# Kernel optimization log

Measured on AMD Instinct MI355X. Metric: run time of the kernel, lower is better.

Reference implementation:

```python
import jax, jax.numpy as jnp
import numpy as np

B, S, DM, NH, WIN = 2, 2048, 1024, 16, 256
DH = DM // NH          # 64
DFF = 4 * DM           # 4096
WIDTHS = (256, 512, 1024)  # 1024 == hidden -> identity (no adapter in torch ModuleDict)


def _ln(x, g, b, eps=1e-5):
    m = jnp.mean(x, -1, keepdims=True)
    v = jnp.var(x, -1, keepdims=True)
    return (x - m) * jax.lax.rsqrt(v + eps) * g + b


def _gelu(t):
    return jax.nn.gelu(t, approximate=False)  # torch nn.GELU default = exact erf


def setup_inputs() -> dict:
    key = jax.random.key(0)
    ks = iter(jax.random.split(key, 32))

    def lin(fi, fo):
        # xavier_uniform(gain=1/sqrt(2)) ~ scale sqrt(2/(fi+fo))/sqrt(2); normal init is fine for a numeric reference
        std = float((1.0 / np.sqrt(2.0)) * np.sqrt(2.0 / (fi + fo)))
        return (jax.random.normal(next(ks), (fi, fo), jnp.float32) * std,
                jnp.zeros((fo,), jnp.float32))

    inp = {}
    inp['x'] = jax.random.normal(next(ks), (B, S, DM), jnp.float32)
    inp['width_multiplier'] = jax.random.uniform(next(ks), (B, S, 1), jnp.float32)
    # attention projections
    inp['wq'], inp['bq'] = lin(DM, DM)
    inp['wk'], inp['bk'] = lin(DM, DM)
    inp['wv'], inp['bv'] = lin(DM, DM)
    inp['wo'], inp['bo'] = lin(DM, DM)
    inp['lnq_g'] = jnp.ones((DH,), jnp.float32); inp['lnq_b'] = jnp.zeros((DH,), jnp.float32)
    inp['lnk_g'] = jnp.ones((DH,), jnp.float32); inp['lnk_b'] = jnp.zeros((DH,), jnp.float32)
    # base FFN
    inp['fc1_w'], inp['fc1_b'] = lin(DM, DFF)
    inp['fc2_w'], inp['fc2_b'] = lin(DFF, DM)
    inp['lni_g'] = jnp.ones((DM,), jnp.float32); inp['lni_b'] = jnp.zeros((DM,), jnp.float32)
    inp['lnh_g'] = jnp.ones((DFF,), jnp.float32); inp['lnh_b'] = jnp.zeros((DFF,), jnp.float32)
    # width adapters (for widths != hidden_dim)
    inp['a256_w1'], inp['a256_b1'] = lin(DM, 256)
    inp['a256_w2'], inp['a256_b2'] = lin(256, DM)
    inp['a512_w1'], inp['a512_b1'] = lin(DM, 512)
    inp['a512_w2'], inp['a512_b2'] = lin(512, DM)
    # router output: index into WIDTHS per token
    inp['width_idx'] = jax.random.randint(next(ks), (B, S), 0, 3)
    return inp


def reference(x, width_multiplier, wq, bq, wk, bk, wv, bv, wo, bo,
              lnq_g, lnq_b, lnk_g, lnk_b, fc1_w, fc1_b, fc2_w, fc2_b,
              lni_g, lni_b, lnh_g, lnh_b,
              a256_w1, a256_b1, a256_w2, a256_b2,
              a512_w1, a512_b1, a512_w2, a512_b2, width_idx):
    # ---- local causal windowed attention pathway ----
    q = (x @ wq + bq).reshape(B, S, NH, DH)
    k = (x @ wk + bk).reshape(B, S, NH, DH)
    v = (x @ wv + bv).reshape(B, S, NH, DH)
    q = _ln(q, lnq_g, lnq_b)  # per-head-dim LayerNorm (torch ln_q on [B,S,H,Dh])
    k = _ln(k, lnk_g, lnk_b)
    scores = jnp.einsum('bihd,bjhd->bhij', q, k) / np.float32(np.sqrt(DH))
    ii = jnp.arange(S)[:, None]
    jj = jnp.arange(S)[None, :]
    allowed = (jj <= ii) & (ii - jj <= WIN)  # causal + local window
    scores = jnp.where(allowed[None, None], scores, -jnp.inf)
    probs = jax.nn.softmax(scores, axis=-1)
    attn = jnp.einsum('bhij,bjhd->bihd', probs, v).reshape(B, S, DM)
    h = x + attn @ wo + bo  # residual around attention pathway

    # ---- width-adaptive FFN ----
    xn = _ln(h, lni_g, lni_b)
    hid = _ln(_gelu(xn @ fc1_w + fc1_b), lnh_g, lnh_b)
    base = hid @ fc2_w + fc2_b
    # per-width adapters, combined by routing mask (dense compute, masked scatter)
    a0 = _gelu(xn @ a256_w1 + a256_b1) @ a256_w2 + a256_b2
    a1 = _gelu(xn @ a512_w1 + a512_b1) @ a512_w2 + a512_b2
    a2 = xn  # width == hidden_dim -> identity pass-through
    m0 = (width_idx == 0)[..., None]
    m1 = (width_idx == 1)[..., None]
    m2 = (width_idx == 2)[..., None]
    adaptive = jnp.where(m0, a0, 0.0) + jnp.where(m1, a1, 0.0) + jnp.where(m2, a2, 0.0)
    ffn_out = base * width_multiplier + adaptive * (1.0 - width_multiplier)
    return h + ffn_out
```

## Files before the change

### kernel.cpp

```cpp
#include <hip/hip_runtime.h>
#include <math.h>

#define B_   2
#define S_   2048
#define DM_  1024
#define NH_  16
#define DH_  64
#define DFF_ 4096
#define WIN_ 256
#define MTOK (B_*S_)

typedef unsigned short ushort_t;
typedef short s16x8 __attribute__((ext_vector_type(8)));
typedef float f32x4 __attribute__((ext_vector_type(4)));

__device__ __forceinline__ float b2f(ushort_t u) {
    union { unsigned int i; float f; } c; c.i = ((unsigned int)u) << 16; return c.f;
}
__device__ __forceinline__ ushort_t f2b(float f) {
    union { float f; unsigned int i; } c; c.f = f;
    unsigned int r = c.i + 0x7fffu + ((c.i >> 16) & 1u);
    return (ushort_t)(r >> 16);
}
__device__ __forceinline__ float gelu_fast(float x) {
    const float u = 0.7978845608f * x * fmaf(0.044715f, x * x, 1.0f);
    const float e = __expf(2.0f * u);
    const float t = 1.0f - 2.0f / (e + 1.0f);
    return 0.5f * x * (1.0f + t);
}
__device__ __forceinline__ void gload16(const void* g, void* l) {
    __builtin_amdgcn_global_load_lds(
        (const __attribute__((address_space(1))) unsigned int*)g,
        (__attribute__((address_space(3))) unsigned int*)l, 16, 0, 0);
}
__device__ __forceinline__ int xcd_swz(int wgid, int nwg) {
    const int nx = 8;
    const int q = nwg / nx, r = nwg % nx;
    const int xcd = wgid % nx, lo = wgid / nx;
    const int base = (xcd < r) ? xcd * (q + 1) : r * (q + 1) + (xcd - r) * q;
    return base + lo;
}

__device__ __forceinline__ void gemm_loop(
    const ushort_t* __restrict__ A, int lda,
    const ushort_t* __restrict__ Bt, int ldb,
    int Kc, int bx, int by, f32x4 (&acc)[4][4])
{
    __shared__ __align__(16) ushort_t As[2][256 * 32];
    __shared__ __align__(16) ushort_t Bs[2][128 * 32];

    const int tid  = threadIdx.x;
    const int lane = tid & 63;
    const int w    = tid >> 6;
    const int row0 = by * 256;
    const int col0 = bx * 128;

    const int srow = lane >> 2;
    const int sk   = (lane & 3) * 8;
    const int wr   = (w >> 1) * 64;
    const int wc   = (w & 1) * 64;
    const int lr   = lane & 15;
    const int lk   = (lane >> 4) * 8;

    auto stage = [&](int buf, int k0) {
        #pragma unroll
        for (int i = 0; i < 2; ++i) {
            const int c = i * 8 + w;
            const int cr = c * 16 + srow;
            gload16(A + (size_t)(row0 + cr) * lda + k0 + sk,
                    (char*)As[buf] + c * 1024);
        }
        {
            const int cr = w * 16 + srow;
            gload16(Bt + (size_t)(col0 + cr) * ldb + k0 + sk,
                    (char*)Bs[buf] + w * 1024);
        }
    };

    const int nk = Kc >> 5;
    stage(0, 0);
    __syncthreads();
    int cur = 0;
    for (int k = 0; k < nk; ++k) {
        if (k + 1 < nk) stage(cur ^ 1, (k + 1) << 5);
        s16x8 af[4], bfr[4];
        #pragma unroll
        for (int mi = 0; mi < 4; ++mi)
            af[mi] = *(const s16x8*)&As[cur][(wr + mi * 16 + lr) * 32 + lk];
        #pragma unroll
        for (int ni = 0; ni < 4; ++ni)
            bfr[ni] = *(const s16x8*)&Bs[cur][(wc + ni * 16 + lr) * 32 + lk];
        #pragma unroll
        for (int mi = 0; mi < 4; ++mi)
            #pragma unroll
            for (int ni = 0; ni < 4; ++ni)
                acc[mi][ni] = __builtin_amdgcn_mfma_f32_16x16x32_bf16(
                    af[mi], bfr[ni], acc[mi][ni], 0, 0, 0);
        __syncthreads();
        cur ^= 1;
    }
}

__global__ __launch_bounds__(512) void gemm_qkvln(
    const ushort_t* __restrict__ A, const ushort_t* __restrict__ Bt,
    const float* __restrict__ bias,
    const float* __restrict__ qg, const float* __restrict__ qb,
    const float* __restrict__ kg, const float* __restrict__ kb,
    ushort_t* __restrict__ qh, ushort_t* __restrict__ kh, ushort_t* __restrict__ vh)
{
    f32x4 acc[4][4] = {};
    gemm_loop(A, 1024, Bt, 1024, 1024, blockIdx.x, blockIdx.y, acc);

    const int lane = threadIdx.x & 63;
    const int w    = threadIdx.x >> 6;
    const int wr   = (w >> 1) * 64;
    const int wc   = (w & 1) * 64;
    const int row0 = blockIdx.y * 256;
    const int col0 = blockIdx.x * 128;
    const int crow = (lane >> 4) * 4;
    const int ccol = lane & 15;
    const int sel  = (col0 + wc) >> 10;
    const int hh   = ((col0 + wc) & 1023) >> 6;
    ushort_t* dst = (sel == 0) ? qh : (sel == 1) ? kh : vh;

    #pragma unroll
    for (int mi = 0; mi < 4; ++mi) {
        float val[4][4];
        float s1[4] = {}, sq[4] = {};
        #pragma unroll
        for (int ni = 0; ni < 4; ++ni) {
            const float bc = bias[col0 + wc + ni * 16 + ccol];
            #pragma unroll
            for (int r = 0; r < 4; ++r) {
                const float v = acc[mi][ni][r] + bc;
                val[ni][r] = v;
                s1[r] += v;
                sq[r] = fmaf(v, v, sq[r]);
            }
        }
        if (sel < 2) {
            #pragma unroll
            for (int r = 0; r < 4; ++r) {
                #pragma unroll
                for (int m = 1; m < 16; m <<= 1) {
                    s1[r] += __shfl_xor(s1[r], m);
                    sq[r] += __shfl_xor(sq[r], m);
                }
            }
        }
        #pragma unroll
        for (int r = 0; r < 4; ++r) {
            const int r_abs = row0 + wr + mi * 16 + crow + r;
            const int bb = r_abs >> 11, ss = r_abs & 2047;
            const size_t db = (((size_t)(bb * NH_ + hh)) * S_ + ss) * 64;
            const float mean = s1[r] * 0.015625f;
            const float var  = sq[r] * 0.015625f - mean * mean;
            const float rstd = rsqrtf(var + 1e-5f);
            #pragma unroll
            for (int ni = 0; ni < 4; ++ni) {
                const int d = ni * 16 + ccol;
                float v = val[ni][r];
                if (sel == 0)      v = ((v - mean) * rstd * qg[d] + qb[d]) * 0.125f;
                else if (sel == 1) v = (v - mean) * rstd * kg[d] + kb[d];
                dst[db + d] = f2b(v);
            }
        }
    }
}

__global__ __launch_bounds__(512) void gemm_fc1ad(
    const ushort_t* __restrict__ A, const ushort_t* __restrict__ Bt,
    const float* __restrict__ bias,
    ushort_t* __restrict__ hid, ushort_t* __restrict__ tA)
{
    f32x4 acc[4][4] = {};
    gemm_loop(A, 1024, Bt, 1024, 1024, blockIdx.x, blockIdx.y, acc);

    const int lane = threadIdx.x & 63;
    const int w    = threadIdx.x >> 6;
    const int wr   = (w >> 1) * 64;
    const int wc   = (w & 1) * 64;
    const int row0 = blockIdx.y * 256;
    const int col0 = blockIdx.x * 128;
    const int crow = (lane >> 4) * 4;
    const int ccol = lane & 15;
    const bool isad = (col0 >= 4096);
    ushort_t* D = isad ? tA : hid;
    const int stride = isad ? 768 : 4096;
    const int cb     = isad ? 4096 : 0;

    #pragma unroll
    for (int ni = 0; ni < 4; ++ni) {
        const int col = col0 + wc + ni * 16 + ccol;
        const float bc = bias[col];
        #pragma unroll
        for (int mi = 0; mi < 4; ++mi) {
            #pragma unroll
            for (int r = 0; r < 4; ++r) {
                const int row = row0 + wr + mi * 16 + crow + r;
                D[(size_t)row * stride + (col - cb)] = f2b(gelu_fast(acc[mi][ni][r] + bc));
            }
        }
    }
}

__device__ __forceinline__ void epi_raw(
    f32x4 (&acc)[4][4], float* __restrict__ C, int N, int bx, int by)
{
    const int lane = threadIdx.x & 63;
    const int w    = threadIdx.x >> 6;
    const int wr   = (w >> 1) * 64;
    const int wc   = (w & 1) * 64;
    const int crow = (lane >> 4) * 4;
    const int ccol = lane & 15;
    #pragma unroll
    for (int ni = 0; ni < 4; ++ni) {
        const int col = bx * 128 + wc + ni * 16 + ccol;
        #pragma unroll
        for (int mi = 0; mi < 4; ++mi) {
            #pragma unroll
            for (int r = 0; r < 4; ++r) {
                const int row = by * 256 + wr + mi * 16 + crow + r;
                C[(size_t)row * N + col] = acc[mi][ni][r];
            }
        }
    }
}

__global__ __launch_bounds__(512) void gemm_wo_sk(
    const ushort_t* __restrict__ A, const ushort_t* __restrict__ Wt,
    float* __restrict__ p0, float* __restrict__ p1)
{
    const int z = blockIdx.z;
    f32x4 acc[4][4] = {};
    gemm_loop(A + z * 512, 1024, Wt + z * 512, 1024, 512, blockIdx.x, blockIdx.y, acc);
    epi_raw(acc, z ? p1 : p0, 1024, blockIdx.x, blockIdx.y);
}

__global__ __launch_bounds__(512) void gemm_fc2_sk(
    const ushort_t* __restrict__ A, const ushort_t* __restrict__ Bt,
    float* __restrict__ p0, float* __restrict__ p1)
{
    const int z = blockIdx.z;
    f32x4 acc[4][4] = {};
    gemm_loop(A + z * 2048, 4096, Bt + z * 2048, 4096, 2048, blockIdx.x, blockIdx.y, acc);
    epi_raw(acc, z ? p1 : p0, 1024, blockIdx.x, blockIdx.y);
}

__global__ __launch_bounds__(512) void gemm_adapters(
    const ushort_t* __restrict__ tA, const ushort_t* __restrict__ w2a,
    const ushort_t* __restrict__ w2b, const float* __restrict__ b2a,
    const float* __restrict__ b2b, float* __restrict__ a0, float* __restrict__ a1)
{
    const int z = blockIdx.z;
    const ushort_t* Ap = z ? tA + 256 : tA;
    const ushort_t* Wp = z ? w2b : w2a;
    const float*    bp = z ? b2b : b2a;
    float*          Cp = z ? a1 : a0;
    const int Kz = z ? 512 : 256;
    f32x4 acc[4][4] = {};
    gemm_loop(Ap, 768, Wp, Kz, Kz, blockIdx.x, blockIdx.y, acc);

    const int lane = threadIdx.x & 63;
    const int w    = threadIdx.x >> 6;
    const int wr   = (w >> 1) * 64;
    const int wc   = (w & 1) * 64;
    const int crow = (lane >> 4) * 4;
    const int ccol = lane & 15;
    #pragma unroll
    for (int ni = 0; ni < 4; ++ni) {
        const int col = blockIdx.x * 128 + wc + ni * 16 + ccol;
        const float bc = bp[col];
        #pragma unroll
        for (int mi = 0; mi < 4; ++mi) {
            #pragma unroll
            for (int r = 0; r < 4; ++r) {
                const int row = blockIdx.y * 256 + wr + mi * 16 + crow + r;
                Cp[(size_t)row * 1024 + col] = acc[mi][ni][r] + bc;
            }
        }
    }
}

__device__ __forceinline__ void wtrans_core(
    const float* __restrict__ W, ushort_t* __restrict__ Wt, int K, int N,
    int bx, int by)
{
    __shared__ float tile[32][33];
    const int n0 = bx * 32, k0 = by * 32;
    const int tx = threadIdx.x & 31, ty = threadIdx.x >> 5;
    #pragma unroll
    for (int j = 0; j < 4; ++j)
        tile[ty + j * 8][tx] = W[(size_t)(k0 + ty + j * 8) * N + n0 + tx];
    __syncthreads();
    #pragma unroll
    for (int j = 0; j < 4; ++j)
        Wt[(size_t)(n0 + ty + j * 8) * K + k0 + tx] = f2b(tile[tx][ty + j * 8]);
}

#define PREP_NBLK 17940
__global__ __launch_bounds__(256) void prep_all(
    const float* wq, const float* wk, const float* wv, const float* wo,
    const float* fc1_w, const float* a256_w1, const float* a512_w1,
    const float* fc2_w, const float* a256_w2, const float* a512_w2,
    const float* bq, const float* bk, const float* bv, const float* fb,
    const float* ab1, const float* ab2,
    const float* x,
    ushort_t* WqkvT, ushort_t* WoT, ushort_t* fc1adT, ushort_t* fc2T,
    ushort_t* w2aT, ushort_t* w2bT,
    float* bqkv, float* bfc1ad, ushort_t* xb)
{
    const int id = blockIdx.x;
    if (id < 4096) {
        const int z = id >> 10, t = id & 1023;
        const float* W = (z == 0) ? wq : (z == 1) ? wk : (z == 2) ? wv : wo;
        ushort_t* D = (z == 3) ? WoT : WqkvT + (size_t)z * 1024 * 1024;
        wtrans_core(W, D, 1024, 1024, t & 31, t >> 5);
    } else if (id < 8192) {
        const int t = id - 4096;
        wtrans_core(fc1_w, fc1adT, 1024, 4096, t & 127, t >> 7);
    } else if (id < 8448) {
        const int t = id - 8192;
        wtrans_core(a256_w1, fc1adT + (size_t)4096 * 1024, 1024, 256, t & 7, t >> 3);
    } else if (id < 8960) {
        const int t = id - 8448;
        wtrans_core(a512_w1, fc1adT + (size_t)4352 * 1024, 1024, 512, t & 15, t >> 4);
    } else if (id < 13056) {
        const int t = id - 8960;
        wtrans_core(fc2_w, fc2T, 4096, 1024, t & 31, t >> 5);
    } else if (id < 13312) {
        const int t = id - 13056;
        wtrans_core(a256_w2, w2aT, 256, 1024, t & 31, t >> 5);
    } else if (id < 13824) {
        const int t = id - 13312;
        wtrans_core(a512_w2, w2bT, 512, 1024, t & 31, t >> 5);
    } else if (id < 13844) {
        const int t = (id - 13824) * 256 + threadIdx.x;
        if (t < 1024) { bqkv[t] = bq[t]; bqkv[1024 + t] = bk[t]; bqkv[2048 + t] = bv[t]; }
        if (t < 4096)      bfc1ad[t] = fb[t];
        else if (t < 4352) bfc1ad[t] = ab1[t - 4096];
        else if (t < 4864) bfc1ad[t] = ab2[t - 4352];
    } else {
        const int i = (id - 13844) * 256 + threadIdx.x;
        float4 v = ((const float4*)x)[i];
        ushort4 o; o.x = f2b(v.x); o.y = f2b(v.y); o.z = f2b(v.z); o.w = f2b(v.w);
        ((ushort4*)xb)[i] = o;
    }
}

__global__ __launch_bounds__(256) void attn_mfma(
    const ushort_t* __restrict__ qh, const ushort_t* __restrict__ kh,
    const ushort_t* __restrict__ vh, ushort_t* __restrict__ o)
{
    __shared__ __align__(16) ushort_t Ks[64 * 64];
    __shared__ __align__(16) ushort_t Vt[64 * 64];
    __shared__ __align__(16) ushort_t Pl[4 * 16 * 64];

    const int bid = xcd_swz(blockIdx.x, gridDim.x);
    const int qt  = bid & 31;
    const int hh  = (bid >> 5) & 15;
    const int b   = bid >> 9;
    const int wq   = threadIdx.x >> 6;
    const int lane = threadIdx.x & 63;
    const int lg  = lane >> 4;
    const int lq  = lane & 15;

    const int i0  = qt * 64;
    const int iw0 = i0 + wq * 16;
    const int i_l = iw0 + lq;

    const size_t plane = ((size_t)(b * NH_ + hh)) * S_ * 64;

    s16x8 qf[2];
    {
        const ushort_t* qp = qh + plane + (size_t)(iw0 + lq) * 64 + lg * 8;
        qf[0] = *(const s16x8*)(qp);
        qf[1] = *(const s16x8*)(qp + 32);
    }

    f32x4 acc[4] = {};
    float M = -1e30f, L = 0.0f;

    const int jstart = (i0 - WIN_) > 0 ? (i0 - WIN_) : 0;
    const int nt     = (i0 + 64 - jstart) >> 6;

    const int srow0 = threadIdx.x >> 3;
    const int sd0   = (threadIdx.x & 7) * 8;

    for (int t = 0; t < nt; ++t) {
        const int j0 = jstart + t * 64;

        #pragma unroll
        for (int pass = 0; pass < 2; ++pass) {
            const int skey = srow0 + pass * 32;
            const size_t src = plane + (size_t)(j0 + skey) * 64 + sd0;
            s16x8 k8 = *(const s16x8*)(kh + src);
            s16x8 v8 = *(const s16x8*)(vh + src);
            *(s16x8*)&Ks[skey * 64 + (sd0 ^ ((skey & 7) << 3))] = k8;
            #pragma unroll
            for (int e = 0; e < 8; ++e) {
                const int d = sd0 + e;
                Vt[d * 64 + (skey ^ (((d >> 1) & 7) << 3))] = (ushort_t)v8[e];
            }
        }
        __syncthreads();

        f32x4 sc[4];
        #pragma unroll
        for (int kt = 0; kt < 4; ++kt) {
            const int krow = kt * 16 + lq;
            const int swk = (krow & 7) << 3;
            s16x8 k0 = *(const s16x8*)&Ks[krow * 64 + ((lg * 8) ^ swk)];
            s16x8 k1 = *(const s16x8*)&Ks[krow * 64 + ((lg * 8 + 32) ^ swk)];
            f32x4 z = {};
            z = __builtin_amdgcn_mfma_f32_16x16x32_bf16(k0, qf[0], z, 0, 0, 0);
            z = __builtin_amdgcn_mfma_f32_16x16x32_bf16(k1, qf[1], z, 0, 0, 0);
            sc[kt] = z;
        }

        const bool fullv = (j0 + 63 <= iw0) && (iw0 + 15 - j0 <= WIN_);
        if (!fullv) {
            #pragma unroll
            for (int kt = 0; kt < 4; ++kt)
                #pragma unroll
                for (int r = 0; r < 4; ++r) {
                    const int jv = j0 + kt * 16 + lg * 4 + r;
                    const int dd = i_l - jv;
                    const bool ok = (dd >= 0) && (dd <= WIN_);
                    sc[kt][r] = ok ? sc[kt][r] : -1e30f;
                }
        }
        float mx = -1e30f;
        #pragma unroll
        for (int kt = 0; kt < 4; ++kt)
            #pragma unroll
            for (int r = 0; r < 4; ++r) mx = fmaxf(mx, sc[kt][r]);
        mx = fmaxf(mx, __shfl_xor(mx, 16));
        mx = fmaxf(mx, __shfl_xor(mx, 32));
        const float nM = fmaxf(M, mx);
        const float alpha = __expf(M - nM);
        M = nM;
        float ts = 0.0f;
        float ev[16];
        #pragma unroll
        for (int kt = 0; kt < 4; ++kt)
            #pragma unroll
            for (int r = 0; r < 4; ++r) {
                float e = __expf(sc[kt][r] - nM);
                if (!fullv) e = (sc[kt][r] > -1e29f) ? e : 0.0f;
                ev[kt * 4 + r] = e;
                ts += e;
            }
        ts += __shfl_xor(ts, 16);
        ts += __shfl_xor(ts, 32);
        L = L * alpha + ts;

        {
            ushort_t* pw = Pl + wq * 1024;
            const int swq = (lq & 7) << 3;
            #pragma unroll
            for (int kt = 0; kt < 4; ++kt)
                #pragma unroll
                for (int pr = 0; pr < 2; ++pr) {
                    const int key0 = kt * 16 + lg * 4 + pr * 2;
                    const unsigned int pk =
                        (unsigned int)f2b(ev[kt * 4 + pr * 2]) |
                        ((unsigned int)f2b(ev[kt * 4 + pr * 2 + 1]) << 16);
                    *(unsigned int*)&pw[lq * 64 + (key0 ^ swq)] = pk;
                }
        }

        float ar[4];
        #pragma unroll
        for (int r = 0; r < 4; ++r) ar[r] = __shfl(alpha, lg * 4 + r);
        #pragma unroll
        for (int dt = 0; dt < 4; ++dt)
            #pragma unroll
            for (int r = 0; r < 4; ++r) acc[dt][r] *= ar[r];

        {
            const ushort_t* pw = Pl + wq * 1024;
            const int swq = (lq & 7) << 3;
            s16x8 pf0 = *(const s16x8*)&pw[lq * 64 + ((lg * 8) ^ swq)];
            s16x8 pf1 = *(const s16x8*)&pw[lq * 64 + ((lg * 8 + 32) ^ swq)];
            #pragma unroll
            for (int dt = 0; dt < 4; ++dt) {
                const int d = dt * 16 + lq;
                const int swd = ((d >> 1) & 7) << 3;
                s16x8 v0 = *(const s16x8*)&Vt[d * 64 + ((lg * 8) ^ swd)];
                s16x8 v1 = *(const s16x8*)&Vt[d * 64 + ((lg * 8 + 32) ^ swd)];
                acc[dt] = __builtin_amdgcn_mfma_f32_16x16x32_bf16(pf0, v0, acc[dt], 0, 0, 0);
                acc[dt] = __builtin_amdgcn_mfma_f32_16x16x32_bf16(pf1, v1, acc[dt], 0, 0, 0);
            }
        }
        __syncthreads();
    }

    const float inv = 1.0f / L;
    float ir[4];
    #pragma unroll
    for (int r = 0; r < 4; ++r) ir[r] = __shfl(inv, lg * 4 + r);
    #pragma unroll
    for (int dt = 0; dt < 4; ++dt)
        #pragma unroll
        for (int r = 0; r < 4; ++r) {
            const int qq = lg * 4 + r;
            o[((size_t)(b * S_ + iw0 + qq)) * DM_ + hh * 64 + dt * 16 + lq] =
                f2b(acc[dt][r] * ir[r]);
        }
}

__global__ __launch_bounds__(256) void ln_token_h(
    const float* __restrict__ p0, const float* __restrict__ p1,
    const float* __restrict__ bo, const float* __restrict__ x,
    float* __restrict__ hb, ushort_t* __restrict__ xnb,
    const float* __restrict__ g, const float* __restrict__ b)
{
    const int t = blockIdx.x;
    const size_t base = (size_t)t * 1024;
    float vals[4];
    float s = 0.0f, s2 = 0.0f;
    #pragma unroll
    for (int i = 0; i < 4; ++i) {
        const int idx = i * 256 + threadIdx.x;
        const float v = x[base + idx] + p0[base + idx] + p1[base + idx] + bo[idx];
        hb[base + idx] = v;
        vals[i] = v;
        s += v;
        s2 = fmaf(v, v, s2);
    }
    #pragma unroll
    for (int o = 32; o >= 1; o >>= 1) { s += __shfl_xor(s, o); s2 += __shfl_xor(s2, o); }
    __shared__ float rs[4], rq[4];
    const int wid = threadIdx.x >> 6, lane = threadIdx.x & 63;
    if (lane == 0) { rs[wid] = s; rq[wid] = s2; }
    __syncthreads();
    s  = rs[0] + rs[1] + rs[2] + rs[3];
    s2 = rq[0] + rq[1] + rq[2] + rq[3];
    const float mean = s * (1.0f / 1024.0f);
    const float var  = s2 * (1.0f / 1024.0f) - mean * mean;
    const float rstd = rsqrtf(var + 1e-5f);
    #pragma unroll
    for (int i = 0; i < 4; ++i) {
        const int idx = i * 256 + threadIdx.x;
        xnb[base + idx] = f2b((vals[i] - mean) * rstd * g[idx] + b[idx]);
    }
}

template <int N>
__global__ __launch_bounds__(256) void ln_token2(
    const ushort_t* __restrict__ in, ushort_t* __restrict__ outp,
    const float* __restrict__ g, const float* __restrict__ b)
{
    constexpr int NPT = N / 256;
    const int t = blockIdx.x;
    const ushort_t* row = in + (size_t)t * N;
    float vals[NPT];
    float s = 0.0f, s2 = 0.0f;
    #pragma unroll
    for (int i = 0; i < NPT; ++i) {
        float x = b2f(row[i * 256 + threadIdx.x]);
        vals[i] = x;
        s += x;
        s2 = fmaf(x, x, s2);
    }
    #pragma unroll
    for (int o = 32; o >= 1; o >>= 1) { s += __shfl_xor(s, o); s2 += __shfl_xor(s2, o); }
    __shared__ float rs[4], rq[4];
    const int wid = threadIdx.x >> 6, lane = threadIdx.x & 63;
    if (lane == 0) { rs[wid] = s; rq[wid] = s2; }
    __syncthreads();
    s  = rs[0] + rs[1] + rs[2] + rs[3];
    s2 = rq[0] + rq[1] + rq[2] + rq[3];
    const float mean = s * (1.0f / N);
    const float var  = s2 * (1.0f / N) - mean * mean;
    const float rstd = rsqrtf(var + 1e-5f);
    #pragma unroll
    for (int i = 0; i < NPT; ++i) {
        const int idx = i * 256 + threadIdx.x;
        outp[(size_t)t * N + idx] = f2b((vals[i] - mean) * rstd * g[idx] + b[idx]);
    }
}

__global__ __launch_bounds__(256) void combine3(
    float* __restrict__ outp, const float* __restrict__ p1,
    const float* __restrict__ fc2b, const float* __restrict__ h,
    const ushort_t* __restrict__ xnb, const float* __restrict__ a0,
    const float* __restrict__ a1, const float* __restrict__ wm,
    const int* __restrict__ widx)
{
    const size_t idx = (size_t)blockIdx.x * 256 + threadIdx.x;
    const int t   = (int)(idx >> 10);
    const int col = (int)(idx & 1023);
    const float w = wm[t];
    const int sel = widx[t];
    const float base = outp[idx] + p1[idx] + fc2b[col];
    const float ad = (sel == 0) ? a0[idx] : ((sel == 1) ? a1[idx] : b2f(xnb[idx]));
    outp[idx] = h[idx] + base * w + ad * (1.0f - w);
}

extern "C" void kernel_launch(void* const* d_in, const int* in_sizes, int n_in,
                              void* d_out, int out_size, void* d_ws, size_t ws_size,
                              hipStream_t stream)
{
    const float* x     = (const float*)d_in[0];
    const float* wm    = (const float*)d_in[1];
    const float* wq    = (const float*)d_in[2];
    const float* bq    = (const float*)d_in[3];
    const float* wk    = (const float*)d_in[4];
    const float* bk    = (const float*)d_in[5];
    const float* wv    = (const float*)d_in[6];
    const float* bv    = (const float*)d_in[7];
    const float* wo    = (const float*)d_in[8];
    const float* bo    = (const float*)d_in[9];
    const float* lnq_g = (const float*)d_in[10];
    const float* lnq_b = (const float*)d_in[11];
    const float* lnk_g = (const float*)d_in[12];
    const float* lnk_b = (const float*)d_in[13];
    const float* fc1_w = (const float*)d_in[14];
    const float* fc1_b = (const float*)d_in[15];
    const float* fc2_w = (const float*)d_in[16];
    const float* fc2_b = (const float*)d_in[17];
    const float* lni_g = (const float*)d_in[18];
    const float* lni_b = (const float*)d_in[19];
    const float* lnh_g = (const float*)d_in[20];
    const float* lnh_b = (const float*)d_in[21];
    const float* a256_w1 = (const float*)d_in[22];
    const float* a256_b1 = (const float*)d_in[23];
    const float* a256_w2 = (const float*)d_in[24];
    const float* a256_b2 = (const float*)d_in[25];
    const float* a512_w1 = (const float*)d_in[26];
    const float* a512_b1 = (const float*)d_in[27];
    const float* a512_w2 = (const float*)d_in[28];
    const float* a512_b2 = (const float*)d_in[29];
    const int*   widx    = (const int*)d_in[30];

    float* out = (float*)d_out;

    char* p = (char*)d_ws;
    auto alloc = [&](size_t bytes) { char* r = p; p += (bytes + 255) & ~(size_t)255; return r; };
    float*    ascr  = (float*)   alloc((size_t)MTOK * 2048 * 4);
    float*    hb    = (float*)   alloc((size_t)MTOK * 1024 * 4);
    ushort_t* xnb   = (ushort_t*)alloc((size_t)MTOK * 1024 * 2);
    ushort_t* hidb  = (ushort_t*)alloc((size_t)MTOK * 4096 * 2);
    ushort_t* tA    = (ushort_t*)alloc((size_t)MTOK * 768 * 2);
    ushort_t* WqkvT = (ushort_t*)alloc((size_t)3072 * 1024 * 2);
    ushort_t* WoT   = (ushort_t*)alloc((size_t)1024 * 1024 * 2);
    ushort_t* fc1adT= (ushort_t*)alloc((size_t)4864 * 1024 * 2);
    ushort_t* fc2T  = (ushort_t*)alloc((size_t)1024 * 4096 * 2);
    ushort_t* w2aT  = (ushort_t*)alloc((size_t)1024 * 256 * 2);
    ushort_t* w2bT  = (ushort_t*)alloc((size_t)1024 * 512 * 2);
    float*    bqkv  = (float*)   alloc(3072 * 4);
    float*    bfc1ad= (float*)   alloc(4864 * 4);
    float*    p1    = (float*)   alloc((size_t)MTOK * 1024 * 4);
    ushort_t* xb    = hidb;
    ushort_t* attnb = hidb + (size_t)MTOK * 1024;
    ushort_t* qh    = hidb + (size_t)MTOK * 2048;
    ushort_t* kh    = hidb + (size_t)MTOK * 3072;
    ushort_t* vh    = (ushort_t*)p1;
    float*    a0    = ascr;
    float*    a1    = ascr + (size_t)MTOK * 1024;

    const dim3 blk(256);
    const dim3 blk512(512);

    prep_all<<<PREP_NBLK, blk, 0, stream>>>(
        wq, wk, wv, wo, fc1_w, a256_w1, a512_w1, fc2_w, a256_w2, a512_w2,
        bq, bk, bv, fc1_b, a256_b1, a512_b1, x,
        WqkvT, WoT, fc1adT, fc2T, w2aT, w2bT, bqkv, bfc1ad, xb);

    gemm_qkvln<<<dim3(24, 16), blk512, 0, stream>>>(xb, WqkvT, bqkv,
        lnq_g, lnq_b, lnk_g, lnk_b, qh, kh, vh);
    attn_mfma<<<B_ * NH_ * (S_ / 64), blk, 0, stream>>>(qh, kh, vh, attnb);

    gemm_wo_sk<<<dim3(8, 16, 2), blk512, 0, stream>>>(attnb, WoT, hb, p1);
    ln_token_h<<<MTOK, blk, 0, stream>>>(hb, p1, bo, x, hb, xnb, lni_g, lni_b);

    gemm_fc1ad<<<dim3(38, 16), blk512, 0, stream>>>(xnb, fc1adT, bfc1ad, hidb, tA);
    ln_token2<DFF_><<<MTOK, blk, 0, stream>>>(hidb, hidb, lnh_g, lnh_b);
    gemm_fc2_sk<<<dim3(8, 16, 2), blk512, 0, stream>>>(hidb, fc2T, out, p1);

    gemm_adapters<<<dim3(8, 16, 2), blk512, 0, stream>>>(tA, w2aT, w2bT,
                                                         a256_b2, a512_b2, a0, a1);

    combine3<<<(int)((size_t)MTOK * 1024 / 256), blk, 0, stream>>>(
        out, p1, fc2_b, hb, xnb, a0, a1, wm, widx);
}
```

Measured before the change: 303.5 us.

## Double GEMM K-tile to 64 with XOR-swizzled LDS and merge fc2/adapter launches

The shared GEMM main loop now stages 64-wide K slices instead of 32, with an XOR swizzle on the LDS column index to avoid bank conflicts, and runs two MFMA sub-steps per barrier. This halves the number of barriers and loop iterations per GEMM. The fc2 split-K kernel and the adapter kernel are merged into one launch with four z-slices so they run concurrently and the adapters fill idle CUs. LDS use doubles to 96 KB per block, which may reduce occupancy.

```diff
diff --git a/kernel.cpp b/kernel.cpp
--- a/kernel.cpp
+++ b/kernel.cpp
@@ -46,8 +46,8 @@
     const ushort_t* __restrict__ Bt, int ldb,
     int Kc, int bx, int by, f32x4 (&acc)[4][4])
 {
-    __shared__ __align__(16) ushort_t As[2][256 * 32];
-    __shared__ __align__(16) ushort_t Bs[2][128 * 32];
+    __shared__ __align__(16) ushort_t As[2][256 * 64];
+    __shared__ __align__(16) ushort_t Bs[2][128 * 64];
 
     const int tid  = threadIdx.x;
     const int lane = tid & 63;
@@ -55,47 +55,56 @@
     const int row0 = by * 256;
     const int col0 = bx * 128;
 
-    const int srow = lane >> 2;
-    const int sk   = (lane & 3) * 8;
+    const int srow = lane >> 3;
+    const int sk   = ((lane & 7) ^ srow) * 8;
     const int wr   = (w >> 1) * 64;
     const int wc   = (w & 1) * 64;
     const int lr   = lane & 15;
-    const int lk   = (lane >> 4) * 8;
+    const int lg   = lane >> 4;
 
     auto stage = [&](int buf, int k0) {
+        #pragma unroll
+        for (int i = 0; i < 4; ++i) {
+            const int c = i * 8 + w;
+            const int cr = c * 8 + srow;
+            gload16(A + (size_t)(row0 + cr) * lda + k0 + sk,
+                    (char*)As[buf] + c * 1024);
+        }
         #pragma unroll
         for (int i = 0; i < 2; ++i) {
             const int c = i * 8 + w;
-            const int cr = c * 16 + srow;
-            gload16(A + (size_t)(row0 + cr) * lda + k0 + sk,
-                    (char*)As[buf] + c * 1024);
-        }
-        {
-            const int cr = w * 16 + srow;
+            const int cr = c * 8 + srow;
             gload16(Bt + (size_t)(col0 + cr) * ldb + k0 + sk,
-                    (char*)Bs[buf] + w * 1024);
+                    (char*)Bs[buf] + c * 1024);
         }
     };
 
-    const int nk = Kc >> 5;
+    const int nk = Kc >> 6;
     stage(0, 0);
     __syncthreads();
     int cur = 0;
     for (int k = 0; k < nk; ++k) {
-        if (k + 1 < nk) stage(cur ^ 1, (k + 1) << 5);
-        s16x8 af[4], bfr[4];
-        #pragma unroll
-        for (int mi = 0; mi < 4; ++mi)
-            af[mi] = *(const s16x8*)&As[cur][(wr + mi * 16 + lr) * 32 + lk];
-        #pragma unroll
-        for (int ni = 0; ni < 4; ++ni)
-            bfr[ni] = *(const s16x8*)&Bs[cur][(wc + ni * 16 + lr) * 32 + lk];
-        #pragma unroll
-        for (int mi = 0; mi < 4; ++mi)
-            #pragma unroll
-            for (int ni = 0; ni < 4; ++ni)
-                acc[mi][ni] = __builtin_amdgcn_mfma_f32_16x16x32_bf16(
-                    af[mi], bfr[ni], acc[mi][ni], 0, 0, 0);
+        if (k + 1 < nk) stage(cur ^ 1, (k + 1) << 6);
+        #pragma unroll
+        for (int ks = 0; ks < 2; ++ks) {
+            s16x8 af[4], bfr[4];
+            #pragma unroll
+            for (int mi = 0; mi < 4; ++mi) {
+                const int r = wr + mi * 16 + lr;
+                af[mi] = *(const s16x8*)&As[cur][r * 64 + (((ks * 4 + lg) ^ (r & 7)) * 8)];
+            }
+            #pragma unroll
+            for (int ni = 0; ni < 4; ++ni) {
+                const int r = wc + ni * 16 + lr;
+                bfr[ni] = *(const s16x8*)&Bs[cur][r * 64 + (((ks * 4 + lg) ^ (r & 7)) * 8)];
+            }
+            #pragma unroll
+            for (int mi = 0; mi < 4; ++mi)
+                #pragma unroll
+                for (int ni = 0; ni < 4; ++ni)
+                    acc[mi][ni] = __builtin_amdgcn_mfma_f32_16x16x32_bf16(
+                        af[mi], bfr[ni], acc[mi][ni], 0, 0, 0);
+        }
         __syncthreads();
         cur ^= 1;
     }
@@ -237,29 +246,25 @@
     epi_raw(acc, z ? p1 : p0, 1024, blockIdx.x, blockIdx.y);
 }
 
-__global__ __launch_bounds__(512) void gemm_fc2_sk(
-    const ushort_t* __restrict__ A, const ushort_t* __restrict__ Bt,
-    float* __restrict__ p0, float* __restrict__ p1)
-{
-    const int z = blockIdx.z;
-    f32x4 acc[4][4] = {};
-    gemm_loop(A + z * 2048, 4096, Bt + z * 2048, 4096, 2048, blockIdx.x, blockIdx.y, acc);
-    epi_raw(acc, z ? p1 : p0, 1024, blockIdx.x, blockIdx.y);
-}
-
-__global__ __launch_bounds__(512) void gemm_adapters(
+__global__ __launch_bounds__(512) void gemm_fc2ad(
+    const ushort_t* __restrict__ hid, const ushort_t* __restrict__ fc2T,
     const ushort_t* __restrict__ tA, const ushort_t* __restrict__ w2a,
     const ushort_t* __restrict__ w2b, const float* __restrict__ b2a,
-    const float* __restrict__ b2b, float* __restrict__ a0, float* __restrict__ a1)
+    const float* __restrict__ b2b,
+    float* __restrict__ p0, float* __restrict__ p1,
+    float* __restrict__ a0, float* __restrict__ a1)
 {
     const int z = blockIdx.z;
-    const ushort_t* Ap = z ? tA + 256 : tA;
-    const ushort_t* Wp = z ? w2b : w2a;
-    const float*    bp = z ? b2b : b2a;
-    float*          Cp = z ? a1 : a0;
-    const int Kz = z ? 512 : 256;
+    const ushort_t* Ap;  const ushort_t* Bp;
+    int lda, Kc;
+    float* Cp;  const float* bp;
+    if (z == 0)      { Ap = hid;        Bp = fc2T;        lda = 4096; Kc = 2048; Cp = p0; bp = nullptr; }
+    else if (z == 1) { Ap = hid + 2048; Bp = fc2T + 2048; lda = 4096; Kc = 2048; Cp = p1; bp = nullptr; }
+    else if (z == 2) { Ap = tA;         Bp = w2a;         lda = 768;  Kc = 256;  Cp = a0; bp = b2a; }
+    else             { Ap = tA + 256;   Bp = w2b;         lda = 768;  Kc = 512;  Cp = a1; bp = b2b; }
+
     f32x4 acc[4][4] = {};
-    gemm_loop(Ap, 768, Wp, Kz, Kz, blockIdx.x, blockIdx.y, acc);
+    gemm_loop(Ap, lda, Bp, (z < 2) ? 4096 : Kc, Kc, blockIdx.x, blockIdx.y, acc);
 
     const int lane = threadIdx.x & 63;
     const int w    = threadIdx.x >> 6;
@@ -270,7 +275,7 @@
     #pragma unroll
     for (int ni = 0; ni < 4; ++ni) {
         const int col = blockIdx.x * 128 + wc + ni * 16 + ccol;
-        const float bc = bp[col];
+        const float bc = bp ? bp[col] : 0.0f;
         #pragma unroll
         for (int mi = 0; mi < 4; ++mi) {
             #pragma unroll
@@ -678,10 +683,9 @@
 
     gemm_fc1ad<<<dim3(38, 16), blk512, 0, stream>>>(xnb, fc1adT, bfc1ad, hidb, tA);
     ln_token2<DFF_><<<MTOK, blk, 0, stream>>>(hidb, hidb, lnh_g, lnh_b);
-    gemm_fc2_sk<<<dim3(8, 16, 2), blk512, 0, stream>>>(hidb, fc2T, out, p1);
-
-    gemm_adapters<<<dim3(8, 16, 2), blk512, 0, stream>>>(tA, w2aT, w2bT,
-                                                         a256_b2, a512_b2, a0, a1);
+
+    gemm_fc2ad<<<dim3(8, 16, 4), blk512, 0, stream>>>(hidb, fc2T, tA, w2aT, w2bT,
+        a256_b2, a512_b2, out, p1, a0, a1);
 
     combine3<<<(int)((size_t)MTOK * 1024 / 256), blk, 0, stream>>>(
         out, p1, fc2_b, hb, xnb, a0, a1, wm, widx);
```

New measurement: 347.5 us. 14.5% more time.

## Swizzle GEMM LDS layout and merge fc2 split-K with adapter GEMMs

Applied to the files above, without the earlier changes.

XOR-swizzles the k-chunk offset used for shared-memory staging and fragment reads in the shared GEMM loop, to cut LDS bank conflicts. It also merges the fc2 split-K GEMM and the two adapter down-projection GEMMs into one launch with four z-slices, saving a launch and letting the short adapter blocks fill idle CUs. The merged grid is load-imbalanced, since adapter slices have K of 256 or 512 against 2048 for fc2. The swizzle has to match the write pattern of the staging loads, or the results will be wrong.

```diff
diff --git a/kernel.cpp b/kernel.cpp
--- a/kernel.cpp
+++ b/kernel.cpp
@@ -56,11 +56,12 @@
     const int col0 = bx * 128;
 
     const int srow = lane >> 2;
-    const int sk   = (lane & 3) * 8;
+    const int sk   = (((lane & 3) ^ ((lane >> 3) & 3)) * 8);
     const int wr   = (w >> 1) * 64;
     const int wc   = (w & 1) * 64;
     const int lr   = lane & 15;
-    const int lk   = (lane >> 4) * 8;
+    const int lg   = lane >> 4;
+    const int lk   = ((lg ^ ((lr >> 1) & 3)) * 8);
 
     auto stage = [&](int buf, int k0) {
         #pragma unroll
@@ -237,29 +238,25 @@
     epi_raw(acc, z ? p1 : p0, 1024, blockIdx.x, blockIdx.y);
 }
 
-__global__ __launch_bounds__(512) void gemm_fc2_sk(
-    const ushort_t* __restrict__ A, const ushort_t* __restrict__ Bt,
-    float* __restrict__ p0, float* __restrict__ p1)
-{
-    const int z = blockIdx.z;
-    f32x4 acc[4][4] = {};
-    gemm_loop(A + z * 2048, 4096, Bt + z * 2048, 4096, 2048, blockIdx.x, blockIdx.y, acc);
-    epi_raw(acc, z ? p1 : p0, 1024, blockIdx.x, blockIdx.y);
-}
-
-__global__ __launch_bounds__(512) void gemm_adapters(
+__global__ __launch_bounds__(512) void gemm_fc2ad(
+    const ushort_t* __restrict__ hid, const ushort_t* __restrict__ fc2T,
     const ushort_t* __restrict__ tA, const ushort_t* __restrict__ w2a,
     const ushort_t* __restrict__ w2b, const float* __restrict__ b2a,
-    const float* __restrict__ b2b, float* __restrict__ a0, float* __restrict__ a1)
+    const float* __restrict__ b2b,
+    float* __restrict__ p0, float* __restrict__ p1,
+    float* __restrict__ a0, float* __restrict__ a1)
 {
     const int z = blockIdx.z;
-    const ushort_t* Ap = z ? tA + 256 : tA;
-    const ushort_t* Wp = z ? w2b : w2a;
-    const float*    bp = z ? b2b : b2a;
-    float*          Cp = z ? a1 : a0;
-    const int Kz = z ? 512 : 256;
+    const ushort_t* Ap;  const ushort_t* Bp;
+    int lda, ldb, Kc;
+    float* Cp;  const float* bp;
+    if (z == 0)      { Ap = hid;        Bp = fc2T;        lda = 4096; ldb = 4096; Kc = 2048; Cp = p0; bp = nullptr; }
+    else if (z == 1) { Ap = hid + 2048; Bp = fc2T + 2048; lda = 4096; ldb = 4096; Kc = 2048; Cp = p1; bp = nullptr; }
+    else if (z == 2) { Ap = tA;         Bp = w2a;         lda = 768;  ldb = 256;  Kc = 256;  Cp = a0; bp = b2a; }
+    else             { Ap = tA + 256;   Bp = w2b;         lda = 768;  ldb = 512;  Kc = 512;  Cp = a1; bp = b2b; }
+
     f32x4 acc[4][4] = {};
-    gemm_loop(Ap, 768, Wp, Kz, Kz, blockIdx.x, blockIdx.y, acc);
+    gemm_loop(Ap, lda, Bp, ldb, Kc, blockIdx.x, blockIdx.y, acc);
 
     const int lane = threadIdx.x & 63;
     const int w    = threadIdx.x >> 6;
@@ -270,7 +267,7 @@
     #pragma unroll
     for (int ni = 0; ni < 4; ++ni) {
         const int col = blockIdx.x * 128 + wc + ni * 16 + ccol;
-        const float bc = bp[col];
+        const float bc = bp ? bp[col] : 0.0f;
         #pragma unroll
         for (int mi = 0; mi < 4; ++mi) {
             #pragma unroll
@@ -678,10 +675,9 @@
 
     gemm_fc1ad<<<dim3(38, 16), blk512, 0, stream>>>(xnb, fc1adT, bfc1ad, hidb, tA);
     ln_token2<DFF_><<<MTOK, blk, 0, stream>>>(hidb, hidb, lnh_g, lnh_b);
-    gemm_fc2_sk<<<dim3(8, 16, 2), blk512, 0, stream>>>(hidb, fc2T, out, p1);
-
-    gemm_adapters<<<dim3(8, 16, 2), blk512, 0, stream>>>(tA, w2aT, w2bT,
-                                                         a256_b2, a512_b2, a0, a1);
+
+    gemm_fc2ad<<<dim3(8, 16, 4), blk512, 0, stream>>>(hidb, fc2T, tA, w2aT, w2bT,
+        a256_b2, a512_b2, out, p1, a0, a1);
 
     combine3<<<(int)((size_t)MTOK * 1024 / 256), blk, 0, stream>>>(
         out, p1, fc2_b, hb, xnb, a0, a1, wm, widx);
```

New measurement: 288.1 us. -5.1%, faster.
